# Performance work log

Measured on AMD Instinct MI355X. Metric: run time of the kernel, lower is better.

## Reference

```python
import jax, jax.numpy as jnp
import numpy as np

N, E = 100000, 400000
IN_C, OUT_C, EA_D = 64, 16, 8


def setup_inputs() -> dict:
    key = jax.random.key(0)
    ks = jax.random.split(key, 12)
    x = jax.random.normal(ks[0], (N, IN_C), dtype=jnp.float32)
    # row (target) indices generated in [1, N] because forward does row -= 1
    row = jax.random.randint(ks[1], (E,), 1, N + 1, dtype=jnp.int32)
    col = jax.random.randint(ks[2], (E,), 0, N, dtype=jnp.int32)
    edge_index = jnp.stack([row, col], axis=0)  # [2, E]
    edge_attr = jax.random.normal(ks[3], (E, EA_D), dtype=jnp.float32)
    s_in = 1.0 / np.sqrt(IN_C)
    s_ea = 1.0 / np.sqrt(EA_D)
    s_o = 1.0 / np.sqrt(OUT_C)
    lin_w = jax.random.uniform(ks[4], (IN_C, OUT_C), jnp.float32, -s_in, s_in)
    lin_b = jax.random.uniform(ks[5], (OUT_C,), jnp.float32, -s_in, s_in)
    ea_w = jax.random.uniform(ks[6], (EA_D, OUT_C), jnp.float32, -s_ea, s_ea)
    ea_b = jax.random.uniform(ks[7], (OUT_C,), jnp.float32, -s_ea, s_ea)
    attn_w1 = jax.random.uniform(ks[8], (OUT_C,), jnp.float32, -1.0, 1.0)  # Linear(1,out)
    attn_b1 = jax.random.uniform(ks[9], (OUT_C,), jnp.float32, -1.0, 1.0)
    attn_w2 = jax.random.uniform(ks[10], (OUT_C,), jnp.float32, -s_o, s_o)  # Linear(out,1)
    attn_b2 = jax.random.uniform(ks[11], (), jnp.float32, -s_o, s_o)
    return {"x": x, "edge_index": edge_index, "edge_attr": edge_attr,
            "lin_w": lin_w, "lin_b": lin_b, "ea_w": ea_w, "ea_b": ea_b,
            "attn_w1": attn_w1, "attn_b1": attn_b1, "attn_w2": attn_w2, "attn_b2": attn_b2}


def reference(x, edge_index, edge_attr, lin_w, lin_b, ea_w, ea_b,
              attn_w1, attn_b1, attn_w2, attn_b2):
    n = x.shape[0]
    h = x @ lin_w + lin_b                      # [N, out]
    row = edge_index[0] - 1                    # forward does row -= 1
    col = edge_index[1]
    ea = edge_attr @ ea_w + ea_b               # [E, out]
    agg = h[col] * ea                          # gather + elementwise  [E, out]
    # attn_mlp: per-scalar Linear(1,out)->ReLU->Linear(out,1) over last dim
    hid = jax.nn.relu(agg[..., None] * attn_w1 + attn_b1)  # [E, out, out]
    scores = hid @ attn_w2 + attn_b2           # [E, out]
    attn = jax.nn.softmax(scores, axis=1)      # softmax over channel dim
    agg = agg * attn
    out = jnp.zeros_like(h).at[row].add(agg)   # scatter_add over target nodes
    return out
```

## Files before the change

kernel.cpp:

```cpp
#include <hip/hip_runtime.h>

#define IN_C 64
#define OUT_C 16
#define EA_D 8

typedef float f32x4 __attribute__((ext_vector_type(4)));

#define DPPF(x, ctrl) \
    __uint_as_float((unsigned)__builtin_amdgcn_update_dpp( \
        0, (int)__float_as_uint(x), (ctrl), 0xF, 0xF, true))

__device__ __forceinline__ void atomic_add_f32(float* p, float v) {
#if defined(__HIP_PLATFORM_AMD__) || defined(__AMDGCN__)
    unsafeAtomicAdd(p, v);
#else
    atomicAdd(p, v);
#endif
}

__global__ __launch_bounds__(256) void h_kernel(
    const float* __restrict__ x,
    const float* __restrict__ lin_w,
    const float* __restrict__ lin_b,
    float* __restrict__ h,
    float* __restrict__ out,
    int n)
{
    __shared__ float s_x [16][IN_C + 4];
    __shared__ float s_wt[16][IN_C + 4];

    const int t = threadIdx.x;
    const int nodeBase = blockIdx.x * 16;

    {
        const int idx = nodeBase * OUT_C + t;
        if (idx < n * OUT_C) out[idx] = 0.0f;
    }

    for (int i = t; i < IN_C * OUT_C; i += 256)
        s_wt[i & 15][i >> 4] = lin_w[i];

    {
        const int lr = t >> 4;
        const int k4 = (t & 15) * 4;
        const int node = nodeBase + lr;
        float4 v = make_float4(0.f, 0.f, 0.f, 0.f);
        if (node < n) v = *(const float4*)(x + (size_t)node * IN_C + k4);
        *(float4*)(&s_x[lr][k4]) = v;
    }
    __syncthreads();

    const int lr = t >> 4;
    const int c  = t & 15;
    const int node = nodeBase + lr;
    if (node < n) {
        float acc = lin_b[c];
        #pragma unroll
        for (int k4 = 0; k4 < IN_C; k4 += 4) {
            const float4 xv = *(const float4*)(&s_x [lr][k4]);
            const float4 wv = *(const float4*)(&s_wt[c ][k4]);
            acc = fmaf(xv.x, wv.x, acc);
            acc = fmaf(xv.y, wv.y, acc);
            acc = fmaf(xv.z, wv.z, acc);
            acc = fmaf(xv.w, wv.w, acc);
        }
        h[(size_t)node * OUT_C + c] = acc;
    }
}

__global__ __launch_bounds__(256) void edge_kernel(
    const int*   __restrict__ edge_index,
    const float* __restrict__ edge_attr,
    const float* __restrict__ ea_w,
    const float* __restrict__ ea_b,
    const float* __restrict__ w1,
    const float* __restrict__ b1,
    const float* __restrict__ w2,
    const float* __restrict__ b2,
    const float* __restrict__ h,
    float*       __restrict__ out,
    int E)
{
    __shared__ float s_eawT[16][12];
    __shared__ float s_eab[OUT_C];

    const int t = threadIdx.x;
    if (t < 128)                s_eawT[t & 15][t >> 4] = ea_w[(t >> 4) * OUT_C + (t & 15)];
    else if (t < 128 + OUT_C)   s_eab[t - 128] = ea_b[t - 128];
    __syncthreads();

    const int gid = blockIdx.x * 256 + t;
    const int e = gid >> 4;
    const int c = gid & 15;
    if (e >= E) return;

    const int row = edge_index[e] - 1;
    const int col = edge_index[E + e];

    const f32x4* ap = (const f32x4*)(edge_attr + (size_t)e * EA_D);
    const f32x4 a0 = ap[0], a1 = ap[1];

    const float hv = h[(size_t)col * OUT_C + c];

    const f32x4 w0 = *(const f32x4*)(&s_eawT[c][0]);
    const f32x4 w4 = *(const f32x4*)(&s_eawT[c][4]);
    float d = s_eab[c];
    d = fmaf(a0.x, w0.x, d);
    d = fmaf(a0.y, w0.y, d);
    d = fmaf(a0.z, w0.z, d);
    d = fmaf(a0.w, w0.w, d);
    d = fmaf(a1.x, w4.x, d);
    d = fmaf(a1.y, w4.y, d);
    d = fmaf(a1.z, w4.z, d);
    d = fmaf(a1.w, w4.w, d);
    const float agg = hv * d;

    float s = b2[0];
    #pragma unroll
    for (int j = 0; j < OUT_C; ++j) {
        const float hm = fmaf(agg, w1[j], b1[j]);
        s = fmaf(fmaxf(hm, 0.0f), w2[j], s);
    }

    float m = s;
    m = fmaxf(m, DPPF(m, 0x140));
    m = fmaxf(m, DPPF(m, 0x141));
    m = fmaxf(m, DPPF(m, 0x4E));
    m = fmaxf(m, DPPF(m, 0xB1));

    const float p = __expf(s - m);
    float den = p;
    den += DPPF(den, 0x140);
    den += DPPF(den, 0x141);
    den += DPPF(den, 0x4E);
    den += DPPF(den, 0xB1);

    const float attn = p * __builtin_amdgcn_rcpf(den);

    atomic_add_f32(out + (size_t)row * OUT_C + c, agg * attn);
}

extern "C" void kernel_launch(void* const* d_in, const int* in_sizes, int n_in,
                              void* d_out, int out_size, void* d_ws, size_t ws_size,
                              hipStream_t stream)
{
    const float* x          = (const float*)d_in[0];
    const int*   edge_index = (const int*)  d_in[1];
    const float* edge_attr  = (const float*)d_in[2];
    const float* lin_w      = (const float*)d_in[3];
    const float* lin_b      = (const float*)d_in[4];
    const float* ea_w       = (const float*)d_in[5];
    const float* ea_b       = (const float*)d_in[6];
    const float* attn_w1    = (const float*)d_in[7];
    const float* attn_b1    = (const float*)d_in[8];
    const float* attn_w2    = (const float*)d_in[9];
    const float* attn_b2    = (const float*)d_in[10];

    const int n = in_sizes[0] / IN_C;
    const int E = in_sizes[1] / 2;

    float* h   = (float*)d_ws;
    float* out = (float*)d_out;

    h_kernel<<<(n + 15) / 16, 256, 0, stream>>>(x, lin_w, lin_b, h, out, n);

    const long long threads = (long long)E * OUT_C;
    edge_kernel<<<(int)((threads + 255) / 256), 256, 0, stream>>>(
        edge_index, edge_attr, ea_w, ea_b,
        attn_w1, attn_b1, attn_w2, attn_b2,
        h, out, E);
}
```

Measured before the change: 128.8 us.

## Register-tile h_kernel over 128 nodes per block with 4x4 outputs per thread

```diff
diff --git a/kernel.cpp b/kernel.cpp
--- a/kernel.cpp
+++ b/kernel.cpp
@@ -18,7 +18,7 @@
 #endif
 }
 
-__global__ __launch_bounds__(256) void h_kernel(
+__global__ __launch_bounds__(128) void h_kernel(
     const float* __restrict__ x,
     const float* __restrict__ lin_w,
     const float* __restrict__ lin_b,
@@ -26,45 +26,73 @@
     float* __restrict__ out,
     int n)
 {
-    __shared__ float s_x [16][IN_C + 4];
+    __shared__ float s_x [128][IN_C + 4];
     __shared__ float s_wt[16][IN_C + 4];
 
     const int t = threadIdx.x;
-    const int nodeBase = blockIdx.x * 16;
+    const int nodeBase = blockIdx.x * 128;
 
     {
-        const int idx = nodeBase * OUT_C + t;
-        if (idx < n * OUT_C) out[idx] = 0.0f;
-    }
-
-    for (int i = t; i < IN_C * OUT_C; i += 256)
+        const int lim = n * OUT_C;
+        #pragma unroll
+        for (int r = 0; r < 4; ++r) {
+            const int idx = nodeBase * OUT_C + (r * 128 + t) * 4;
+            if (idx < lim) *(f32x4*)(out + idx) = (f32x4){0.f, 0.f, 0.f, 0.f};
+        }
+    }
+
+    #pragma unroll
+    for (int i = t; i < IN_C * OUT_C; i += 128)
         s_wt[i & 15][i >> 4] = lin_w[i];
 
-    {
-        const int lr = t >> 4;
-        const int k4 = (t & 15) * 4;
-        const int node = nodeBase + lr;
-        float4 v = make_float4(0.f, 0.f, 0.f, 0.f);
-        if (node < n) v = *(const float4*)(x + (size_t)node * IN_C + k4);
-        *(float4*)(&s_x[lr][k4]) = v;
+    #pragma unroll
+    for (int r = 0; r < 16; ++r) {
+        const int i = r * 128 + t;
+        const int nd = i >> 4;
+        const int k4 = (i & 15) * 4;
+        const int node = nodeBase + nd;
+        f32x4 v = {0.f, 0.f, 0.f, 0.f};
+        if (node < n) v = *(const f32x4*)(x + (size_t)node * IN_C + k4);
+        *(f32x4*)(&s_x[nd][k4]) = v;
     }
     __syncthreads();
 
-    const int lr = t >> 4;
-    const int c  = t & 15;
-    const int node = nodeBase + lr;
-    if (node < n) {
-        float acc = lin_b[c];
-        #pragma unroll
-        for (int k4 = 0; k4 < IN_C; k4 += 4) {
-            const float4 xv = *(const float4*)(&s_x [lr][k4]);
-            const float4 wv = *(const float4*)(&s_wt[c ][k4]);
-            acc = fmaf(xv.x, wv.x, acc);
-            acc = fmaf(xv.y, wv.y, acc);
-            acc = fmaf(xv.z, wv.z, acc);
-            acc = fmaf(xv.w, wv.w, acc);
+    const int ng = t >> 2;
+    const int c0 = (t & 3) * 4;
+
+    float acc[4][4];
+    #pragma unroll
+    for (int m = 0; m < 4; ++m)
+        #pragma unroll
+        for (int j = 0; j < 4; ++j)
+            acc[m][j] = lin_b[c0 + j];
+
+    #pragma unroll
+    for (int k4 = 0; k4 < IN_C; k4 += 4) {
+        f32x4 wv[4];
+        #pragma unroll
+        for (int j = 0; j < 4; ++j)
+            wv[j] = *(const f32x4*)(&s_wt[c0 + j][k4]);
+        #pragma unroll
+        for (int m = 0; m < 4; ++m) {
+            const f32x4 xv = *(const f32x4*)(&s_x[ng + m * 32][k4]);
+            #pragma unroll
+            for (int j = 0; j < 4; ++j) {
+                acc[m][j] = fmaf(xv.x, wv[j].x, acc[m][j]);
+                acc[m][j] = fmaf(xv.y, wv[j].y, acc[m][j]);
+                acc[m][j] = fmaf(xv.z, wv[j].z, acc[m][j]);
+                acc[m][j] = fmaf(xv.w, wv[j].w, acc[m][j]);
+            }
         }
-        h[(size_t)node * OUT_C + c] = acc;
+    }
+
+    #pragma unroll
+    for (int m = 0; m < 4; ++m) {
+        const int node = nodeBase + ng + m * 32;
+        if (node < n) {
+            f32x4 res = {acc[m][0], acc[m][1], acc[m][2], acc[m][3]};
+            *(f32x4*)(h + (size_t)node * OUT_C + c0) = res;
+        }
     }
 }
 
@@ -162,7 +190,7 @@
     float* h   = (float*)d_ws;
     float* out = (float*)d_out;
 
-    h_kernel<<<(n + 15) / 16, 256, 0, stream>>>(x, lin_w, lin_b, h, out, n);
+    h_kernel<<<(n + 127) / 128, 128, 0, stream>>>(x, lin_w, lin_b, h, out, n);
 
     const long long threads = (long long)E * OUT_C;
     edge_kernel<<<(int)((threads + 255) / 256), 256, 0, stream>>>(
```

Result: slower. 140.1 us (+8.7%).

## Register-tile h_kernel to 64 nodes per block with 2x2 outputs per thread

Applied to the files above, without the earlier changes.

```diff
diff --git a/kernel.cpp b/kernel.cpp
--- a/kernel.cpp
+++ b/kernel.cpp
@@ -5,6 +5,7 @@
 #define EA_D 8
 
 typedef float f32x4 __attribute__((ext_vector_type(4)));
+typedef float f32x2 __attribute__((ext_vector_type(2)));
 
 #define DPPF(x, ctrl) \
     __uint_as_float((unsigned)__builtin_amdgcn_update_dpp( \
@@ -26,45 +27,67 @@
     float* __restrict__ out,
     int n)
 {
-    __shared__ float s_x [16][IN_C + 4];
+    __shared__ float s_x [64][IN_C + 4];
     __shared__ float s_wt[16][IN_C + 4];
 
     const int t = threadIdx.x;
-    const int nodeBase = blockIdx.x * 16;
+    const int nodeBase = blockIdx.x * 64;
 
     {
-        const int idx = nodeBase * OUT_C + t;
-        if (idx < n * OUT_C) out[idx] = 0.0f;
+        const int idx = nodeBase * OUT_C + t * 4;
+        if (idx < n * OUT_C) *(f32x4*)(out + idx) = (f32x4){0.f, 0.f, 0.f, 0.f};
     }
 
+    #pragma unroll
     for (int i = t; i < IN_C * OUT_C; i += 256)
         s_wt[i & 15][i >> 4] = lin_w[i];
 
-    {
-        const int lr = t >> 4;
-        const int k4 = (t & 15) * 4;
-        const int node = nodeBase + lr;
-        float4 v = make_float4(0.f, 0.f, 0.f, 0.f);
-        if (node < n) v = *(const float4*)(x + (size_t)node * IN_C + k4);
-        *(float4*)(&s_x[lr][k4]) = v;
+    #pragma unroll
+    for (int r = 0; r < 4; ++r) {
+        const int i  = r * 256 + t;
+        const int nd = i >> 4;
+        const int k4 = (i & 15) * 4;
+        const int node = nodeBase + nd;
+        f32x4 v = {0.f, 0.f, 0.f, 0.f};
+        if (node < n) v = *(const f32x4*)(x + (size_t)node * IN_C + k4);
+        *(f32x4*)(&s_x[nd][k4]) = v;
     }
     __syncthreads();
 
-    const int lr = t >> 4;
-    const int c  = t & 15;
-    const int node = nodeBase + lr;
-    if (node < n) {
-        float acc = lin_b[c];
-        #pragma unroll
-        for (int k4 = 0; k4 < IN_C; k4 += 4) {
-            const float4 xv = *(const float4*)(&s_x [lr][k4]);
-            const float4 wv = *(const float4*)(&s_wt[c ][k4]);
-            acc = fmaf(xv.x, wv.x, acc);
-            acc = fmaf(xv.y, wv.y, acc);
-            acc = fmaf(xv.z, wv.z, acc);
-            acc = fmaf(xv.w, wv.w, acc);
+    const int ng = t >> 3;
+    const int c0 = (t & 7) * 2;
+
+    float a00 = lin_b[c0], a01 = lin_b[c0 + 1];
+    float a10 = lin_b[c0], a11 = lin_b[c0 + 1];
+
+    #pragma unroll
+    for (int k4 = 0; k4 < IN_C; k4 += 4) {
+        const f32x4 w0 = *(const f32x4*)(&s_wt[c0    ][k4]);
+        const f32x4 w1 = *(const f32x4*)(&s_wt[c0 + 1][k4]);
+        const f32x4 x0 = *(const f32x4*)(&s_x[ng     ][k4]);
+        const f32x4 x1 = *(const f32x4*)(&s_x[ng + 32][k4]);
+
+        a00 = fmaf(x0.x, w0.x, a00); a00 = fmaf(x0.y, w0.y, a00);
+        a00 = fmaf(x0.z, w0.z, a00); a00 = fmaf(x0.w, w0.w, a00);
+        a01 = fmaf(x0.x, w1.x, a01); a01 = fmaf(x0.y, w1.y, a01);
+        a01 = fmaf(x0.z, w1.z, a01); a01 = fmaf(x0.w, w1.w, a01);
+        a10 = fmaf(x1.x, w0.x, a10); a10 = fmaf(x1.y, w0.y, a10);
+        a10 = fmaf(x1.z, w0.z, a10); a10 = fmaf(x1.w, w0.w, a10);
+        a11 = fmaf(x1.x, w1.x, a11); a11 = fmaf(x1.y, w1.y, a11);
+        a11 = fmaf(x1.z, w1.z, a11); a11 = fmaf(x1.w, w1.w, a11);
+    }
+
+    {
+        const int node0 = nodeBase + ng;
+        if (node0 < n) {
+            f32x2 r = {a00, a01};
+            *(f32x2*)(h + (size_t)node0 * OUT_C + c0) = r;
         }
-        h[(size_t)node * OUT_C + c] = acc;
+        const int node1 = nodeBase + ng + 32;
+        if (node1 < n) {
+            f32x2 r = {a10, a11};
+            *(f32x2*)(h + (size_t)node1 * OUT_C + c0) = r;
+        }
     }
 }
 
@@ -162,7 +185,7 @@
     float* h   = (float*)d_ws;
     float* out = (float*)d_out;
 
-    h_kernel<<<(n + 15) / 16, 256, 0, stream>>>(x, lin_w, lin_b, h, out, n);
+    h_kernel<<<(n + 63) / 64, 256, 0, stream>>>(x, lin_w, lin_b, h, out, n);
 
     const long long threads = (long long)E * OUT_C;
     edge_kernel<<<(int)((threads + 255) / 256), 256, 0, stream>>>(
```

Measured after the change: 141.0 us. 9.4% more time.
